# Performance work log

Measured on AMD Instinct MI355X. Metric: run time of the kernel, lower is better.

Reference implementation:

```python
import jax, jax.numpy as jnp
import numpy as np

R = 5                       # kernels_radius
D = 2 * R + 1               # kernels_diameter
KERNELS_DESC = [
    {"weight": 0.9, "xy": 6.0, "image": 0.1},
    {"weight": 0.1, "xy": 6.0},
]


def _unfold(t, r):
    """torch F.unfold with padding=r, stride=1 -> [N, C, D, D, H, W]."""
    N, C, H, W = t.shape
    d = 2 * r + 1
    tp = jnp.pad(t, ((0, 0), (0, 0), (r, r), (r, r)))
    # fixed small loop over D*D kernel offsets (121), not over data dims
    pats = jnp.stack(
        [tp[:, :, i:i + H, j:j + W] for i in range(d) for j in range(d)],
        axis=2,
    )
    return pats.reshape(N, C, d, d, H, W)


def reference(x, y_hat):
    N, _, H, W = x.shape
    dt = x.dtype
    # xy coordinate feature [N, 2, H, W]: (col index, row index)
    cols = jnp.broadcast_to(jnp.arange(W, dtype=dt)[None, :], (H, W))
    rows = jnp.broadcast_to(jnp.arange(H, dtype=dt)[:, None], (H, W))
    xy = jnp.broadcast_to(jnp.stack([cols, rows], 0)[None], (N, 2, H, W))

    kernels = jnp.zeros((N, 1, D, D, H, W), dtype=dt)
    for desc in KERNELS_DESC:
        feats = []
        for modality, sigma in desc.items():
            if modality == 'weight':
                continue
            f = xy if modality == 'xy' else x
            feats.append(f / sigma)
        features = jnp.concatenate(feats, axis=1)          # [N, c, H, W]
        k = _unfold(features, R)                           # [N, c, D, D, H, W]
        k = k - k[:, :, R, R][:, :, None, None]            # diff to window center
        k = jnp.exp((-0.5 * k ** 2).sum(axis=1, keepdims=True))
        k = k.at[:, :, R, R].set(0.0)                      # zero self-affinity
        kernels = kernels + desc['weight'] * k

    Cy = y_hat.shape[1]
    yu = _unfold(y_hat, R)                                  # [N, Cy, D, D, H, W]
    prod = (kernels * yu).reshape(N, Cy, D * D, H, W).sum(axis=2)
    loss = kernels.sum() - (prod * y_hat).sum()
    denom = jnp.asarray(N * H * W, dtype=dt)
    return loss / denom


def setup_inputs() -> dict:
    key = jax.random.key(0)
    k1, k2 = jax.random.split(key)
    x = jax.random.normal(k1, (4, 3, 128, 128), dtype=jnp.float32)
    y_hat = jax.random.uniform(k2, (4, 21, 128, 128), dtype=jnp.float32)
    return {"x": x, "y_hat": y_hat}
```

## Files before the change

kernel.cpp:

```cpp
#include <hip/hip_runtime.h>

constexpr int IMG_H = 128;
constexpr int IMG_W = 128;
constexpr int N_IMG = 4;
constexpr int CXCH = 3;
constexpr int CYCH = 21;
constexpr int RAD = 5;
constexpr int DIA = 11;
constexpr int TILE_H = 8;
constexpr int TILE_W = 16;
constexpr int PT_H = TILE_H + 2 * RAD;
constexpr int PT_W = TILE_W + 2 * RAD;
constexpr int NPIX = PT_H * PT_W;
constexpr int NPIXT = TILE_H * TILE_W;
constexpr int NGROUP = 4;
constexpr int NTHREADS = NPIXT * NGROUP;
constexpr int NPAIR = 60;
constexpr int PPG = NPAIR / NGROUP;
constexpr int HW = IMG_H * IMG_W;

__global__ __launch_bounds__(NTHREADS, 4)
void gcrf_kernel(const float* __restrict__ x, const float* __restrict__ y,
                 float* __restrict__ out) {
    __shared__ __align__(16) float sy[NPIX * 20];
    __shared__ __align__(16) float sx[NPIX * 4];
    __shared__ int   s_pk[NPAIR];
    __shared__ float s_e1[NPAIR];
    __shared__ float s_red[NTHREADS / 64];

    const int tid = threadIdx.x;
    const int n = blockIdx.z;
    const int h0 = blockIdx.y * TILE_H;
    const int w0 = blockIdx.x * TILE_W;

    const float* xb = x + (size_t)n * CXCH * HW;
    const float* yb = y + (size_t)n * CYCH * HW;

    if (tid < NPAIR) {
        int di, dj;
        if (tid < 5) { di = 0; dj = tid + 1; }
        else         { int m = tid - 5; di = 1 + m / 11; dj = m % 11 - 5; }
        s_pk[tid] = (di << 8) | (dj + 8);
        s_e1[tid] = __expf(-0.5f * (float)(di * di + dj * dj) * (1.0f / 36.0f));
    }

    for (int p = tid; p < NPIX; p += NTHREADS) {
        int ti = p / PT_W, tj = p - ti * PT_W;
        int gh = h0 + ti - RAD, gw = w0 + tj - RAD;
        bool inb = ((unsigned)gh < (unsigned)IMG_H) && ((unsigned)gw < (unsigned)IMG_W);
        int gofs = gh * IMG_W + gw;
        float v[CYCH];
        #pragma unroll
        for (int c = 0; c < CYCH; c++) v[c] = inb ? yb[c * HW + gofs] : 0.0f;
        float xv[CXCH];
        #pragma unroll
        for (int c = 0; c < CXCH; c++) xv[c] = inb ? xb[c * HW + gofs] : 0.0f;
        #pragma unroll
        for (int q = 0; q < 5; q++) {
            *(float4*)&sy[p * 20 + q * 4] =
                make_float4(v[q * 4 + 0], v[q * 4 + 1], v[q * 4 + 2], v[q * 4 + 3]);
        }
        *(float4*)&sx[p * 4] = make_float4(xv[0], xv[1], xv[2], v[20]);
    }
    __syncthreads();

    const int g = tid >> 7;
    const int pix = tid & (NPIXT - 1);
    const int tx = pix & (TILE_W - 1);
    const int ty = pix >> 4;
    const int h = h0 + ty, w = w0 + tx;
    const int cp = (ty + RAD) * PT_W + (tx + RAD);

    const float4 cx4 = *(const float4*)&sx[cp * 4];
    float yc[20];
    #pragma unroll
    for (int q = 0; q < 5; q++) {
        float4 t = *(const float4*)&sy[cp * 20 + q * 4];
        yc[q * 4 + 0] = t.x; yc[q * 4 + 1] = t.y;
        yc[q * 4 + 2] = t.z; yc[q * 4 + 3] = t.w;
    }

    float acc = 0.0f;
    if (g == 0) {
        int i0 = max(0, RAD - h), i1 = min(DIA - 1, IMG_H - 1 - h + RAD);
        int j0 = max(0, RAD - w), j1 = min(DIA - 1, IMG_W - 1 - w + RAD);
        int n_oob = DIA * DIA - (i1 - i0 + 1) * (j1 - j0 + 1);
        if (n_oob > 0) {
            float oxy = (float)(h * h + w * w) * (1.0f / 36.0f);
            float s2c = cx4.x * cx4.x + cx4.y * cx4.y + cx4.z * cx4.z;
            float kvo = __expf(-0.5f * oxy) * (0.9f * __expf(-50.0f * s2c) + 0.1f);
            acc = (float)n_oob * kvo;
        }
    }

    float accp = 0.0f;
    #pragma unroll
    for (int t = 0; t < PPG; t++) {
        int k = g * PPG + t;
        int pk = s_pk[k];
        float e1 = s_e1[k];
        int di = pk >> 8, dj = (pk & 255) - 8;
        int p = cp + di * PT_W + dj;
        float4 xq = *(const float4*)&sx[p * 4];
        float dot = xq.w * cx4.w;
        #pragma unroll
        for (int q = 0; q < 5; q++) {
            float4 tt = *(const float4*)&sy[p * 20 + q * 4];
            dot += tt.x * yc[q * 4 + 0] + tt.y * yc[q * 4 + 1] +
                   tt.z * yc[q * 4 + 2] + tt.w * yc[q * 4 + 3];
        }
        float d0 = xq.x - cx4.x, d1 = xq.y - cx4.y, d2 = xq.z - cx4.z;
        float s2 = d0 * d0 + d1 * d1 + d2 * d2;
        bool inb = ((h + di) < IMG_H) && ((unsigned)(w + dj) < (unsigned)IMG_W);
        float e = inb ? e1 : 0.0f;
        float kv = e * (0.9f * __expf(-50.0f * s2) + 0.1f);
        accp += kv * (1.0f - dot);
    }

    float total = acc + 2.0f * accp;

    #pragma unroll
    for (int s = 32; s > 0; s >>= 1) total += __shfl_down(total, s, 64);
    if ((tid & 63) == 0) s_red[tid >> 6] = total;
    __syncthreads();
    if (tid == 0) {
        float bs = 0.0f;
        #pragma unroll
        for (int wv = 0; wv < NTHREADS / 64; wv++) bs += s_red[wv];
        atomicAdd(out, bs * (1.0f / (float)(N_IMG * HW)));
    }
}

extern "C" void kernel_launch(void* const* d_in, const int* in_sizes, int n_in,
                              void* d_out, int out_size, void* d_ws, size_t ws_size,
                              hipStream_t stream) {
    const float* x = (const float*)d_in[0];
    const float* y = (const float*)d_in[1];
    float* out = (float*)d_out;
    hipMemsetAsync(out, 0, sizeof(float), stream);
    dim3 grid(IMG_W / TILE_W, IMG_H / TILE_H, N_IMG);
    gcrf_kernel<<<grid, NTHREADS, 0, stream>>>(x, y, out);
}
```

Before: 76.78 us.

## Compute two adjacent pixels per thread sharing neighbor loads, one row offset per wave

Each thread now handles two horizontally adjacent center pixels and reuses each loaded neighbor's 24 floats for both pair terms. Work is split by row offset, one wave per di in 0..5, instead of by pair index, which also removes the shared pair-table lookups. Shared memory is merged into a single 28-float-stride interleaved layout. The cost is fewer threads per block (384) and more registers per thread for two center vectors.

Result: slower. 79.00 us (+2.9%).

```diff
diff --git a/kernel.cpp b/kernel.cpp
--- a/kernel.cpp
+++ b/kernel.cpp
@@ -12,21 +12,32 @@
 constexpr int PT_H = TILE_H + 2 * RAD;
 constexpr int PT_W = TILE_W + 2 * RAD;
 constexpr int NPIX = PT_H * PT_W;
-constexpr int NPIXT = TILE_H * TILE_W;
-constexpr int NGROUP = 4;
-constexpr int NTHREADS = NPIXT * NGROUP;
-constexpr int NPAIR = 60;
-constexpr int PPG = NPAIR / NGROUP;
+constexpr int PSTR = 28;
+constexpr int NWAVES = 6;
+constexpr int NTHREADS = NWAVES * 64;
 constexpr int HW = IMG_H * IMG_W;
 
-__global__ __launch_bounds__(NTHREADS, 4)
+__device__ __forceinline__ float pair_term(
+    const float* __restrict__ yc, const float* __restrict__ xc,
+    const float4 q0, const float4 q1, const float4 q2,
+    const float4 q3, const float4 q4, const float4 q5, float e1) {
+    float dot = q5.x * yc[20];
+    dot += q0.x * yc[0]  + q0.y * yc[1]  + q0.z * yc[2]  + q0.w * yc[3];
+    dot += q1.x * yc[4]  + q1.y * yc[5]  + q1.z * yc[6]  + q1.w * yc[7];
+    dot += q2.x * yc[8]  + q2.y * yc[9]  + q2.z * yc[10] + q2.w * yc[11];
+    dot += q3.x * yc[12] + q3.y * yc[13] + q3.z * yc[14] + q3.w * yc[15];
+    dot += q4.x * yc[16] + q4.y * yc[17] + q4.z * yc[18] + q4.w * yc[19];
+    float d0 = q5.y - xc[0], d1 = q5.z - xc[1], d2 = q5.w - xc[2];
+    float s2 = d0 * d0 + d1 * d1 + d2 * d2;
+    float kv = e1 * (0.9f * __expf(-50.0f * s2) + 0.1f);
+    return kv * (1.0f - dot);
+}
+
+__global__ __launch_bounds__(NTHREADS, 3)
 void gcrf_kernel(const float* __restrict__ x, const float* __restrict__ y,
                  float* __restrict__ out) {
-    __shared__ __align__(16) float sy[NPIX * 20];
-    __shared__ __align__(16) float sx[NPIX * 4];
-    __shared__ int   s_pk[NPAIR];
-    __shared__ float s_e1[NPAIR];
-    __shared__ float s_red[NTHREADS / 64];
+    __shared__ __align__(16) float s[NPIX * PSTR];
+    __shared__ float s_red[NWAVES];
 
     const int tid = threadIdx.x;
     const int n = blockIdx.z;
@@ -36,18 +47,11 @@
     const float* xb = x + (size_t)n * CXCH * HW;
     const float* yb = y + (size_t)n * CYCH * HW;
 
-    if (tid < NPAIR) {
-        int di, dj;
-        if (tid < 5) { di = 0; dj = tid + 1; }
-        else         { int m = tid - 5; di = 1 + m / 11; dj = m % 11 - 5; }
-        s_pk[tid] = (di << 8) | (dj + 8);
-        s_e1[tid] = __expf(-0.5f * (float)(di * di + dj * dj) * (1.0f / 36.0f));
-    }
-
     for (int p = tid; p < NPIX; p += NTHREADS) {
         int ti = p / PT_W, tj = p - ti * PT_W;
         int gh = h0 + ti - RAD, gw = w0 + tj - RAD;
-        bool inb = ((unsigned)gh < (unsigned)IMG_H) && ((unsigned)gw < (unsigned)IMG_W);
+        bool inb = ((unsigned)gh < (unsigned)IMG_H) &&
+                   ((unsigned)gw < (unsigned)IMG_W);
         int gofs = gh * IMG_W + gw;
         float v[CYCH];
         #pragma unroll
@@ -55,78 +59,119 @@
         float xv[CXCH];
         #pragma unroll
         for (int c = 0; c < CXCH; c++) xv[c] = inb ? xb[c * HW + gofs] : 0.0f;
+        float* d = &s[p * PSTR];
         #pragma unroll
-        for (int q = 0; q < 5; q++) {
-            *(float4*)&sy[p * 20 + q * 4] =
-                make_float4(v[q * 4 + 0], v[q * 4 + 1], v[q * 4 + 2], v[q * 4 + 3]);
-        }
-        *(float4*)&sx[p * 4] = make_float4(xv[0], xv[1], xv[2], v[20]);
+        for (int q = 0; q < 5; q++)
+            *(float4*)&d[q * 4] = make_float4(v[q * 4 + 0], v[q * 4 + 1],
+                                              v[q * 4 + 2], v[q * 4 + 3]);
+        *(float4*)&d[20] = make_float4(v[20], xv[0], xv[1], xv[2]);
     }
     __syncthreads();
 
-    const int g = tid >> 7;
-    const int pix = tid & (NPIXT - 1);
-    const int tx = pix & (TILE_W - 1);
-    const int ty = pix >> 4;
-    const int h = h0 + ty, w = w0 + tx;
-    const int cp = (ty + RAD) * PT_W + (tx + RAD);
+    const int g = tid >> 6;
+    const int lane = tid & 63;
+    const int row = lane >> 3;
+    const int cs = lane & 7;
+    const int h = h0 + row;
+    const int wA = w0 + cs * 2;
+    const int cp = (row + RAD) * PT_W + (cs * 2 + RAD);
 
-    const float4 cx4 = *(const float4*)&sx[cp * 4];
-    float yc[20];
-    #pragma unroll
-    for (int q = 0; q < 5; q++) {
-        float4 t = *(const float4*)&sy[cp * 20 + q * 4];
-        yc[q * 4 + 0] = t.x; yc[q * 4 + 1] = t.y;
-        yc[q * 4 + 2] = t.z; yc[q * 4 + 3] = t.w;
+    float ycA[CYCH], ycB[CYCH], xcA[CXCH], xcB[CXCH];
+    {
+        const float* a = &s[cp * PSTR];
+        const float* b = a + PSTR;
+        #pragma unroll
+        for (int q = 0; q < 5; q++) {
+            float4 t = *(const float4*)&a[q * 4];
+            ycA[q * 4 + 0] = t.x; ycA[q * 4 + 1] = t.y;
+            ycA[q * 4 + 2] = t.z; ycA[q * 4 + 3] = t.w;
+            float4 u = *(const float4*)&b[q * 4];
+            ycB[q * 4 + 0] = u.x; ycB[q * 4 + 1] = u.y;
+            ycB[q * 4 + 2] = u.z; ycB[q * 4 + 3] = u.w;
+        }
+        float4 t = *(const float4*)&a[20];
+        ycA[20] = t.x; xcA[0] = t.y; xcA[1] = t.z; xcA[2] = t.w;
+        float4 u = *(const float4*)&b[20];
+        ycB[20] = u.x; xcB[0] = u.y; xcB[1] = u.z; xcB[2] = u.w;
     }
 
-    float acc = 0.0f;
+    const int di = g;
+    const bool rowok = (h + di) < IMG_H;
+    const float erow = __expf(-(float)(di * di) * (1.0f / 72.0f));
+    const float EDJ[6] = {1.0f, 0.98620695f, 0.94595945f,
+                          0.88249690f, 0.80073744f, 0.70664826f};
+
+    float acco = 0.0f;
+    float accp = 0.0f;
+
     if (g == 0) {
-        int i0 = max(0, RAD - h), i1 = min(DIA - 1, IMG_H - 1 - h + RAD);
-        int j0 = max(0, RAD - w), j1 = min(DIA - 1, IMG_W - 1 - w + RAD);
-        int n_oob = DIA * DIA - (i1 - i0 + 1) * (j1 - j0 + 1);
-        if (n_oob > 0) {
-            float oxy = (float)(h * h + w * w) * (1.0f / 36.0f);
-            float s2c = cx4.x * cx4.x + cx4.y * cx4.y + cx4.z * cx4.z;
-            float kvo = __expf(-0.5f * oxy) * (0.9f * __expf(-50.0f * s2c) + 0.1f);
-            acc = (float)n_oob * kvo;
+        #pragma unroll
+        for (int i = 0; i < 2; i++) {
+            int ww = wA + i;
+            const float* xc = i ? xcB : xcA;
+            int i0 = max(0, RAD - h), i1 = min(DIA - 1, IMG_H - 1 - h + RAD);
+            int j0 = max(0, RAD - ww), j1 = min(DIA - 1, IMG_W - 1 - ww + RAD);
+            int n_oob = DIA * DIA - (i1 - i0 + 1) * (j1 - j0 + 1);
+            if (n_oob > 0) {
+                float oxy = (float)(h * h + ww * ww) * (1.0f / 36.0f);
+                float s2c = xc[0] * xc[0] + xc[1] * xc[1] + xc[2] * xc[2];
+                float kvo = __expf(-0.5f * oxy) *
+                            (0.9f * __expf(-50.0f * s2c) + 0.1f);
+                acco += (float)n_oob * kvo;
+            }
+        }
+        #pragma unroll
+        for (int j = 6; j < 12; j++) {
+            const float* nb = &s[(cp + (j - 5)) * PSTR];
+            float4 q0 = *(const float4*)&nb[0];
+            float4 q1 = *(const float4*)&nb[4];
+            float4 q2 = *(const float4*)&nb[8];
+            float4 q3 = *(const float4*)&nb[12];
+            float4 q4 = *(const float4*)&nb[16];
+            float4 q5 = *(const float4*)&nb[20];
+            int gc = wA + (j - 5);
+            float f = ((unsigned)gc < (unsigned)IMG_W) ? 1.0f : 0.0f;
+            if (j <= 10)
+                accp += pair_term(ycA, xcA, q0, q1, q2, q3, q4, q5,
+                                  f * EDJ[j - 5]);
+            if (j >= 7)
+                accp += pair_term(ycB, xcB, q0, q1, q2, q3, q4, q5,
+                                  f * EDJ[j - 6]);
+        }
+    } else {
+        #pragma unroll
+        for (int j = 0; j < 12; j++) {
+            const float* nb = &s[(cp + di * PT_W + (j - 5)) * PSTR];
+            float4 q0 = *(const float4*)&nb[0];
+            float4 q1 = *(const float4*)&nb[4];
+            float4 q2 = *(const float4*)&nb[8];
+            float4 q3 = *(const float4*)&nb[12];
+            float4 q4 = *(const float4*)&nb[16];
+            float4 q5 = *(const float4*)&nb[20];
+            int gc = wA + (j - 5);
+            float f = (rowok && (unsigned)gc < (unsigned)IMG_W) ? erow : 0.0f;
+            if (j <= 10) {
+                int a = j >= 5 ? j - 5 : 5 - j;
+                accp += pair_term(ycA, xcA, q0, q1, q2, q3, q4, q5, f * EDJ[a]);
+            }
+            if (j >= 1) {
+                int a = j >= 6 ? j - 6 : 6 - j;
+                accp += pair_term(ycB, xcB, q0, q1, q2, q3, q4, q5, f * EDJ[a]);
+            }
         }
     }
 
-    float accp = 0.0f;
-    #pragma unroll
-    for (int t = 0; t < PPG; t++) {
-        int k = g * PPG + t;
-        int pk = s_pk[k];
-        float e1 = s_e1[k];
-        int di = pk >> 8, dj = (pk & 255) - 8;
-        int p = cp + di * PT_W + dj;
-        float4 xq = *(const float4*)&sx[p * 4];
-        float dot = xq.w * cx4.w;
-        #pragma unroll
-        for (int q = 0; q < 5; q++) {
-            float4 tt = *(const float4*)&sy[p * 20 + q * 4];
-            dot += tt.x * yc[q * 4 + 0] + tt.y * yc[q * 4 + 1] +
-                   tt.z * yc[q * 4 + 2] + tt.w * yc[q * 4 + 3];
-        }
-        float d0 = xq.x - cx4.x, d1 = xq.y - cx4.y, d2 = xq.z - cx4.z;
-        float s2 = d0 * d0 + d1 * d1 + d2 * d2;
-        bool inb = ((h + di) < IMG_H) && ((unsigned)(w + dj) < (unsigned)IMG_W);
-        float e = inb ? e1 : 0.0f;
-        float kv = e * (0.9f * __expf(-50.0f * s2) + 0.1f);
-        accp += kv * (1.0f - dot);
-    }
-
-    float total = acc + 2.0f * accp;
+    float total = acco + 2.0f * accp;
 
     #pragma unroll
-    for (int s = 32; s > 0; s >>= 1) total += __shfl_down(total, s, 64);
-    if ((tid & 63) == 0) s_red[tid >> 6] = total;
+    for (int sft = 32; sft > 0; sft >>= 1)
+        total += __shfl_down(total, sft, 64);
+    if (lane == 0) s_red[g] = total;
     __syncthreads();
     if (tid == 0) {
         float bs = 0.0f;
         #pragma unroll
-        for (int wv = 0; wv < NTHREADS / 64; wv++) bs += s_red[wv];
+        for (int wv = 0; wv < NWAVES; wv++) bs += s_red[wv];
         atomicAdd(out, bs * (1.0f / (float)(N_IMG * HW)));
     }
 }
```
